# Optimization experiments

Measured on AMD Instinct MI355X. Metric: run time of the kernel, lower is better.

Reference implementation:

```python
import jax, jax.numpy as jnp
import numpy as np

THRESH_FACTOR = 0.7

def _bitlinear(x, w, scale):
    # Ternary quantization of weights: sign(w) masked by |w| > mean(|w|)*0.7,
    # STE in torch means forward value == wq; scale is per-output-row.
    w_abs = jnp.abs(w)
    thr = jnp.mean(w_abs) * THRESH_FACTOR
    wq = jnp.sign(w) * (w_abs > thr).astype(w.dtype)
    w_scaled = wq * scale  # [out, in]
    return jnp.einsum('bsd,od->bso', x, w_scaled)

def setup_inputs() -> dict:
    key = jax.random.key(0)
    k1, k2, k3, k4 = jax.random.split(key, 4)
    dim, hidden = 4096, 16384
    x = jax.random.normal(k1, (2, 2048, dim), dtype=jnp.float32)
    gate_w = jax.random.normal(k2, (hidden, dim), dtype=jnp.float32) / np.sqrt(dim)
    up_w = jax.random.normal(k3, (hidden, dim), dtype=jnp.float32) / np.sqrt(dim)
    down_w = jax.random.normal(k4, (dim, hidden), dtype=jnp.float32) / np.sqrt(hidden)
    return {
        'x': x,
        'gate_w': gate_w, 'gate_scale': jnp.ones((hidden, 1), jnp.float32),
        'up_w': up_w, 'up_scale': jnp.ones((hidden, 1), jnp.float32),
        'down_w': down_w, 'down_scale': jnp.ones((dim, 1), jnp.float32),
    }

def reference(x, gate_w, gate_scale, up_w, up_scale, down_w, down_scale):
    gate = _bitlinear(x, gate_w, gate_scale)      # [B,S,hidden]
    up = _bitlinear(x, up_w, up_scale)            # [B,S,hidden]
    hidden = jax.nn.silu(gate) * up
    out = _bitlinear(hidden, down_w, down_scale)  # [B,S,dim]
    # FakeQuantActivation with bits=8 is an exact identity (bits >= 8 branch)
    return out
```

## Files before the change

kernel.cpp:

```cpp
#include <hip/hip_runtime.h>

typedef __attribute__((ext_vector_type(8))) short short8;
typedef __attribute__((ext_vector_type(4))) float f32x4;

#define AS1 __attribute__((address_space(1)))
#define AS3 __attribute__((address_space(3)))

__device__ __forceinline__ void async_cp16(void* lds_dst, const void* g_src) {
  __builtin_amdgcn_global_load_lds((const AS1 void*)g_src, (AS3 void*)lds_dst, 16, 0, 0);
}

__device__ __forceinline__ unsigned short f2bf(float f) {
  unsigned int x = __float_as_uint(f);
  x += 0x7FFFu + ((x >> 16) & 1u);
  return (unsigned short)(x >> 16);
}

__global__ void k_absmean(const float4* __restrict__ w, int n4, double* __restrict__ out) {
  double s = 0.0;
  int stride = gridDim.x * blockDim.x;
  for (int i = blockIdx.x * blockDim.x + threadIdx.x; i < n4; i += stride) {
    float4 v = w[i];
    s += (double)(fabsf(v.x) + fabsf(v.y) + fabsf(v.z) + fabsf(v.w));
  }
  for (int off = 32; off > 0; off >>= 1) s += __shfl_down(s, off);
  __shared__ double ss[4];
  int lane = threadIdx.x & 63, wid = threadIdx.x >> 6;
  if (lane == 0) ss[wid] = s;
  __syncthreads();
  if (threadIdx.x == 0) atomicAdd(out, ss[0] + ss[1] + ss[2] + ss[3]);
}

__global__ void k_quant_w_dense(const float* __restrict__ w, unsigned short* __restrict__ dst,
                                int nchunks, const double* __restrict__ sum, double inv_n) {
  float thr = (float)(*sum * 0.7 * inv_n);
  int stride = gridDim.x * blockDim.x;
  const float4* w4 = (const float4*)w;
  for (int c = blockIdx.x * blockDim.x + threadIdx.x; c < nchunks; c += stride) {
    float4 a = w4[(size_t)c * 2], b = w4[(size_t)c * 2 + 1];
    float v[8] = {a.x, a.y, a.z, a.w, b.x, b.y, b.z, b.w};
    short8 o;
#pragma unroll
    for (int e = 0; e < 8; e++) {
      unsigned int bits = __float_as_uint(v[e]);
      unsigned short q = (fabsf(v[e]) > thr)
                             ? (unsigned short)(0x3F80u | ((bits >> 16) & 0x8000u))
                             : (unsigned short)0;
      o[e] = (short)q;
    }
    *(short8*)(dst + (size_t)c * 8) = o;
  }
}

__global__ void k_quant_w_inplace(float* __restrict__ w, int nchunks,
                                  const double* __restrict__ sum, double inv_n) {
  float thr = (float)(*sum * 0.7 * inv_n);
  int stride = gridDim.x * blockDim.x;
  for (int c = blockIdx.x * blockDim.x + threadIdx.x; c < nchunks; c += stride) {
    const float4* src = (const float4*)((const char*)w + (size_t)c * 32);
    float4 a = src[0], b = src[1];
    float v[8] = {a.x, a.y, a.z, a.w, b.x, b.y, b.z, b.w};
    short8 o;
#pragma unroll
    for (int e = 0; e < 8; e++) {
      unsigned int bits = __float_as_uint(v[e]);
      unsigned short q = (fabsf(v[e]) > thr)
                             ? (unsigned short)(0x3F80u | ((bits >> 16) & 0x8000u))
                             : (unsigned short)0;
      o[e] = (short)q;
    }
    *(short8*)((char*)w + (size_t)c * 32) = o;
  }
}

__global__ void k_quant_x(const float4* __restrict__ x, unsigned short* __restrict__ xq,
                          int nchunks) {
  int stride = gridDim.x * blockDim.x;
  for (int c = blockIdx.x * blockDim.x + threadIdx.x; c < nchunks; c += stride) {
    float4 a = x[(size_t)c * 2], b = x[(size_t)c * 2 + 1];
    float v[8] = {a.x, a.y, a.z, a.w, b.x, b.y, b.z, b.w};
    short8 o;
#pragma unroll
    for (int e = 0; e < 8; e++) o[e] = (short)f2bf(v[e]);
    *(short8*)(xq + (size_t)c * 8) = o;
  }
}

__global__ __launch_bounds__(256, 2) void k_mlp_gemm1(
    const char* __restrict__ xq, const char* __restrict__ gw, const char* __restrict__ uw,
    const float* __restrict__ gscale, const float* __restrict__ uscale,
    unsigned short* __restrict__ hidden, size_t bRow, int bChunk, int bStep) {
  __shared__ __align__(16) unsigned short sA[4096], sG[4096], sU[4096];
  const int tid = threadIdx.x, lane = tid & 63, wid = tid >> 6;
  const int mt = blockIdx.x & 31, nt = blockIdx.x >> 5;
  const size_t m0 = (size_t)mt * 128, n0 = (size_t)nt * 128;

  const int q0 = wid * 64 + lane, q1 = q0 + 256;
  const int r0 = q0 >> 2, c0 = (q0 & 3) ^ ((q0 >> 3) & 3);
  const int r1 = q1 >> 2, c1 = (q1 & 3) ^ ((q1 >> 3) & 3);

  const char* srcA0 = xq + (m0 + r0) * 8192 + c0 * 16;
  const char* srcA1 = xq + (m0 + r1) * 8192 + c1 * 16;
  const char* srcG0 = gw + (n0 + r0) * bRow + (size_t)c0 * bChunk;
  const char* srcG1 = gw + (n0 + r1) * bRow + (size_t)c1 * bChunk;
  const char* srcU0 = uw + (n0 + r0) * bRow + (size_t)c0 * bChunk;
  const char* srcU1 = uw + (n0 + r1) * bRow + (size_t)c1 * bChunk;

  char* dA0 = (char*)sA + wid * 1024; char* dA1 = dA0 + 4096;
  char* dG0 = (char*)sG + wid * 1024; char* dG1 = dG0 + 4096;
  char* dU0 = (char*)sU + wid * 1024; char* dU1 = dU0 + 4096;

  const int wm = wid >> 1, wn = wid & 1, ln = lane & 15;
  const int slot = ((lane >> 4) ^ ((ln >> 1) & 3)) * 16;
  const char* aBase = (const char*)sA + (size_t)(wm * 64 + ln) * 64 + slot;
  const char* gBase = (const char*)sG + (size_t)(wn * 64 + ln) * 64 + slot;
  const char* uBase = (const char*)sU + (size_t)(wn * 64 + ln) * 64 + slot;

  f32x4 accg[4][4] = {}; f32x4 accu[4][4] = {};

  for (int kt = 0; kt < 4096; kt += 32) {
    async_cp16(dA0, srcA0); async_cp16(dA1, srcA1);
    async_cp16(dG0, srcG0); async_cp16(dG1, srcG1);
    async_cp16(dU0, srcU0); async_cp16(dU1, srcU1);
    srcA0 += 64; srcA1 += 64;
    srcG0 += bStep; srcG1 += bStep; srcU0 += bStep; srcU1 += bStep;
    __syncthreads();
    short8 a[4], bg[4], bu[4];
#pragma unroll
    for (int i = 0; i < 4; i++) {
      a[i]  = *(const short8*)(aBase + i * 1024);
      bg[i] = *(const short8*)(gBase + i * 1024);
      bu[i] = *(const short8*)(uBase + i * 1024);
    }
#pragma unroll
    for (int i = 0; i < 4; i++)
#pragma unroll
      for (int j = 0; j < 4; j++) {
        accg[i][j] = __builtin_amdgcn_mfma_f32_16x16x32_bf16(a[i], bg[j], accg[i][j], 0, 0, 0);
        accu[i][j] = __builtin_amdgcn_mfma_f32_16x16x32_bf16(a[i], bu[j], accu[i][j], 0, 0, 0);
      }
    __syncthreads();
  }

  const int rgrp = lane >> 4;
#pragma unroll
  for (int j = 0; j < 4; j++) {
    int n = (int)n0 + wn * 64 + j * 16 + ln;
    float gs = gscale[n], us = uscale[n];
#pragma unroll
    for (int i = 0; i < 4; i++) {
      int rowb = (int)m0 + wm * 64 + i * 16 + rgrp * 4;
#pragma unroll
      for (int r = 0; r < 4; r++) {
        float g = accg[i][j][r] * gs;
        float u = accu[i][j][r] * us;
        float h = g * (1.0f / (1.0f + __expf(-g))) * u;
        hidden[(size_t)(rowb + r) * 16384 + n] = f2bf(h);
      }
    }
  }
}

__global__ __launch_bounds__(256, 3) void k_mlp_gemm2(
    const char* __restrict__ hq, const char* __restrict__ dw,
    const float* __restrict__ dscale, float* __restrict__ out,
    size_t bRow, int bChunk, int bStep) {
  __shared__ __align__(16) unsigned short sA[4096], sB[4096];
  const int tid = threadIdx.x, lane = tid & 63, wid = tid >> 6;
  const int mt = blockIdx.x & 31, nt = blockIdx.x >> 5;
  const size_t m0 = (size_t)mt * 128, n0 = (size_t)nt * 128;

  const int q0 = wid * 64 + lane, q1 = q0 + 256;
  const int r0 = q0 >> 2, c0 = (q0 & 3) ^ ((q0 >> 3) & 3);
  const int r1 = q1 >> 2, c1 = (q1 & 3) ^ ((q1 >> 3) & 3);

  const char* srcA0 = hq + (m0 + r0) * 32768 + c0 * 16;
  const char* srcA1 = hq + (m0 + r1) * 32768 + c1 * 16;
  const char* srcB0 = dw + (n0 + r0) * bRow + (size_t)c0 * bChunk;
  const char* srcB1 = dw + (n0 + r1) * bRow + (size_t)c1 * bChunk;

  char* dA0 = (char*)sA + wid * 1024; char* dA1 = dA0 + 4096;
  char* dB0 = (char*)sB + wid * 1024; char* dB1 = dB0 + 4096;

  const int wm = wid >> 1, wn = wid & 1, ln = lane & 15;
  const int slot = ((lane >> 4) ^ ((ln >> 1) & 3)) * 16;
  const char* aBase = (const char*)sA + (size_t)(wm * 64 + ln) * 64 + slot;
  const char* bBase = (const char*)sB + (size_t)(wn * 64 + ln) * 64 + slot;

  f32x4 acc[4][4] = {};

  for (int kt = 0; kt < 16384; kt += 32) {
    async_cp16(dA0, srcA0); async_cp16(dA1, srcA1);
    async_cp16(dB0, srcB0); async_cp16(dB1, srcB1);
    srcA0 += 64; srcA1 += 64; srcB0 += bStep; srcB1 += bStep;
    __syncthreads();
    short8 a[4], b[4];
#pragma unroll
    for (int i = 0; i < 4; i++) {
      a[i] = *(const short8*)(aBase + i * 1024);
      b[i] = *(const short8*)(bBase + i * 1024);
    }
#pragma unroll
    for (int i = 0; i < 4; i++)
#pragma unroll
      for (int j = 0; j < 4; j++)
        acc[i][j] = __builtin_amdgcn_mfma_f32_16x16x32_bf16(a[i], b[j], acc[i][j], 0, 0, 0);
    __syncthreads();
  }

  const int rgrp = lane >> 4;
#pragma unroll
  for (int j = 0; j < 4; j++) {
    int n = (int)n0 + wn * 64 + j * 16 + ln;
    float ds = dscale[n];
#pragma unroll
    for (int i = 0; i < 4; i++) {
      int rowb = (int)m0 + wm * 64 + i * 16 + rgrp * 4;
#pragma unroll
      for (int r = 0; r < 4; r++)
        out[(size_t)(rowb + r) * 4096 + n] = acc[i][j][r] * ds;
    }
  }
}

extern "C" void kernel_launch(void* const* d_in, const int* in_sizes, int n_in,
                              void* d_out, int out_size, void* d_ws, size_t ws_size,
                              hipStream_t stream) {
  (void)in_sizes; (void)n_in; (void)out_size;
  const float* x      = (const float*)d_in[0];
  float*       gate_w = (float*)d_in[1];
  const float* gscale = (const float*)d_in[2];
  float*       up_w   = (float*)d_in[3];
  const float* uscale = (const float*)d_in[4];
  float*       down_w = (float*)d_in[5];
  const float* dscale = (const float*)d_in[6];
  float*       out    = (float*)d_out;

  const size_t MB128 = 134217728ull;
  const bool dense = ws_size >= 4 * MB128 + 24;
  unsigned short* hidden = (unsigned short*)d_ws;
  unsigned short* gq = (unsigned short*)((char*)d_ws + 1 * MB128);
  unsigned short* uq = (unsigned short*)((char*)d_ws + 2 * MB128);
  unsigned short* dq = (unsigned short*)((char*)d_ws + 3 * MB128);
  double* sums = (double*)((char*)d_ws + (dense ? 4 * MB128 : MB128));
  unsigned short* xq = (unsigned short*)d_out;

  hipMemsetAsync(sums, 0, 3 * sizeof(double), stream);
  k_absmean<<<4096, 256, 0, stream>>>((const float4*)gate_w, 16777216, sums + 0);
  k_absmean<<<4096, 256, 0, stream>>>((const float4*)up_w,   16777216, sums + 1);
  k_absmean<<<4096, 256, 0, stream>>>((const float4*)down_w, 16777216, sums + 2);

  const double inv_n = 1.0 / 67108864.0;
  k_quant_x<<<2048, 256, 0, stream>>>((const float4*)x, xq, 2097152);

  if (dense) {
    k_quant_w_dense<<<4096, 256, 0, stream>>>(gate_w, gq, 8388608, sums + 0, inv_n);
    k_quant_w_dense<<<4096, 256, 0, stream>>>(up_w,   uq, 8388608, sums + 1, inv_n);
    k_quant_w_dense<<<4096, 256, 0, stream>>>(down_w, dq, 8388608, sums + 2, inv_n);
    k_mlp_gemm1<<<4096, 256, 0, stream>>>((const char*)xq, (const char*)gq, (const char*)uq,
                                          gscale, uscale, hidden, 8192, 16, 64);
    k_mlp_gemm2<<<1024, 256, 0, stream>>>((const char*)hidden, (const char*)dq,
                                          dscale, out, 32768, 16, 64);
  } else {
    k_quant_w_inplace<<<4096, 256, 0, stream>>>(gate_w, 8388608, sums + 0, inv_n);
    k_quant_w_inplace<<<4096, 256, 0, stream>>>(up_w,   8388608, sums + 1, inv_n);
    k_quant_w_inplace<<<4096, 256, 0, stream>>>(down_w, 8388608, sums + 2, inv_n);
    k_mlp_gemm1<<<4096, 256, 0, stream>>>((const char*)xq, (const char*)gate_w,
                                          (const char*)up_w, gscale, uscale, hidden,
                                          16384, 32, 128);
    k_mlp_gemm2<<<1024, 256, 0, stream>>>((const char*)hidden, (const char*)down_w,
                                          dscale, out, 65536, 32, 128);
  }
}
```

Before: 2.760 ms.

## Pipeline GEMMs with 4-stage LDS ring, 8-wave blocks, merge prep kernels

Both GEMMs now use 512-thread blocks with a 128KB four-slot LDS ring buffer, so global-to-LDS async copies run two k-steps ahead. Split barriers with s_waitcnt and s_setprio let MFMA work overlap with loads. Tile shapes grow (gemm1 256x128, gemm2 256x256) and block IDs are swizzled for L2 locality. The separate absmean and quantization kernels are merged into two launches to cut launch overhead. In exchange, the large LDS footprint limits occupancy and raises register pressure, and the hand-tuned waitcnt counts are fragile.

```diff
diff --git a/kernel.cpp b/kernel.cpp
--- a/kernel.cpp
+++ b/kernel.cpp
@@ -6,7 +6,7 @@
 #define AS1 __attribute__((address_space(1)))
 #define AS3 __attribute__((address_space(3)))
 
-__device__ __forceinline__ void async_cp16(void* lds_dst, const void* g_src) {
+__device__ __forceinline__ void async_cp16(char* lds_dst, const char* g_src) {
   __builtin_amdgcn_global_load_lds((const AS1 void*)g_src, (AS3 void*)lds_dst, 16, 0, 0);
 }
 
@@ -16,10 +16,13 @@
   return (unsigned short)(x >> 16);
 }
 
-__global__ void k_absmean(const float4* __restrict__ w, int n4, double* __restrict__ out) {
+__global__ void k_sums(const float4* __restrict__ w0, const float4* __restrict__ w1,
+                       const float4* __restrict__ w2, double* __restrict__ out) {
+  const int seg = blockIdx.x >> 12, bid = blockIdx.x & 4095;
+  const float4* w = (seg == 0) ? w0 : (seg == 1) ? w1 : w2;
   double s = 0.0;
-  int stride = gridDim.x * blockDim.x;
-  for (int i = blockIdx.x * blockDim.x + threadIdx.x; i < n4; i += stride) {
+  const int stride = 4096 * 256;
+  for (int i = bid * 256 + threadIdx.x; i < 16777216; i += stride) {
     float4 v = w[i];
     s += (double)(fabsf(v.x) + fabsf(v.y) + fabsf(v.z) + fabsf(v.w));
   }
@@ -28,199 +31,251 @@
   int lane = threadIdx.x & 63, wid = threadIdx.x >> 6;
   if (lane == 0) ss[wid] = s;
   __syncthreads();
-  if (threadIdx.x == 0) atomicAdd(out, ss[0] + ss[1] + ss[2] + ss[3]);
-}
-
-__global__ void k_quant_w_dense(const float* __restrict__ w, unsigned short* __restrict__ dst,
-                                int nchunks, const double* __restrict__ sum, double inv_n) {
-  float thr = (float)(*sum * 0.7 * inv_n);
-  int stride = gridDim.x * blockDim.x;
-  const float4* w4 = (const float4*)w;
-  for (int c = blockIdx.x * blockDim.x + threadIdx.x; c < nchunks; c += stride) {
-    float4 a = w4[(size_t)c * 2], b = w4[(size_t)c * 2 + 1];
-    float v[8] = {a.x, a.y, a.z, a.w, b.x, b.y, b.z, b.w};
-    short8 o;
-#pragma unroll
-    for (int e = 0; e < 8; e++) {
-      unsigned int bits = __float_as_uint(v[e]);
-      unsigned short q = (fabsf(v[e]) > thr)
-                             ? (unsigned short)(0x3F80u | ((bits >> 16) & 0x8000u))
-                             : (unsigned short)0;
-      o[e] = (short)q;
-    }
-    *(short8*)(dst + (size_t)c * 8) = o;
-  }
-}
-
-__global__ void k_quant_w_inplace(float* __restrict__ w, int nchunks,
-                                  const double* __restrict__ sum, double inv_n) {
-  float thr = (float)(*sum * 0.7 * inv_n);
-  int stride = gridDim.x * blockDim.x;
-  for (int c = blockIdx.x * blockDim.x + threadIdx.x; c < nchunks; c += stride) {
-    const float4* src = (const float4*)((const char*)w + (size_t)c * 32);
-    float4 a = src[0], b = src[1];
-    float v[8] = {a.x, a.y, a.z, a.w, b.x, b.y, b.z, b.w};
-    short8 o;
-#pragma unroll
-    for (int e = 0; e < 8; e++) {
-      unsigned int bits = __float_as_uint(v[e]);
-      unsigned short q = (fabsf(v[e]) > thr)
-                             ? (unsigned short)(0x3F80u | ((bits >> 16) & 0x8000u))
-                             : (unsigned short)0;
-      o[e] = (short)q;
-    }
-    *(short8*)((char*)w + (size_t)c * 32) = o;
-  }
-}
-
-__global__ void k_quant_x(const float4* __restrict__ x, unsigned short* __restrict__ xq,
-                          int nchunks) {
-  int stride = gridDim.x * blockDim.x;
-  for (int c = blockIdx.x * blockDim.x + threadIdx.x; c < nchunks; c += stride) {
-    float4 a = x[(size_t)c * 2], b = x[(size_t)c * 2 + 1];
-    float v[8] = {a.x, a.y, a.z, a.w, b.x, b.y, b.z, b.w};
-    short8 o;
-#pragma unroll
-    for (int e = 0; e < 8; e++) o[e] = (short)f2bf(v[e]);
-    *(short8*)(xq + (size_t)c * 8) = o;
-  }
-}
-
-__global__ __launch_bounds__(256, 2) void k_mlp_gemm1(
+  if (threadIdx.x == 0) atomicAdd(out + seg, ss[0] + ss[1] + ss[2] + ss[3]);
+}
+
+__global__ void k_prep(const float4* __restrict__ x, unsigned short* __restrict__ xq,
+                       float* __restrict__ w0, float* __restrict__ w1, float* __restrict__ w2,
+                       unsigned short* __restrict__ d0, unsigned short* __restrict__ d1,
+                       unsigned short* __restrict__ d2,
+                       const double* __restrict__ sums, double inv_n, int dense) {
+  const int seg = blockIdx.x >> 12;
+  if (seg < 3) {
+    float* w = (seg == 0) ? w0 : (seg == 1) ? w1 : w2;
+    unsigned short* dst = (seg == 0) ? d0 : (seg == 1) ? d1 : d2;
+    const float thr = (float)(sums[seg] * 0.7 * inv_n);
+    const int bid = blockIdx.x & 4095, stride = 4096 * 256;
+    for (int c = bid * 256 + threadIdx.x; c < 8388608; c += stride) {
+      float4 a, b;
+      if (dense) {
+        const float4* w4 = (const float4*)w;
+        a = w4[(size_t)c * 2]; b = w4[(size_t)c * 2 + 1];
+      } else {
+        const float4* src = (const float4*)((const char*)w + (size_t)c * 32);
+        a = src[0]; b = src[1];
+      }
+      float v[8] = {a.x, a.y, a.z, a.w, b.x, b.y, b.z, b.w};
+      short8 o;
+#pragma unroll
+      for (int e = 0; e < 8; e++) {
+        unsigned int bits = __float_as_uint(v[e]);
+        unsigned short q = (fabsf(v[e]) > thr)
+                               ? (unsigned short)(0x3F80u | ((bits >> 16) & 0x8000u))
+                               : (unsigned short)0;
+        o[e] = (short)q;
+      }
+      if (dense) *(short8*)(dst + (size_t)c * 8) = o;
+      else       *(short8*)((char*)w + (size_t)c * 32) = o;
+    }
+  } else {
+    const int bid = blockIdx.x & 4095, stride = 1024 * 256;
+    for (int c = bid * 256 + threadIdx.x; c < 2097152; c += stride) {
+      float4 a = x[(size_t)c * 2], b = x[(size_t)c * 2 + 1];
+      float v[8] = {a.x, a.y, a.z, a.w, b.x, b.y, b.z, b.w};
+      short8 o;
+#pragma unroll
+      for (int e = 0; e < 8; e++) o[e] = (short)f2bf(v[e]);
+      *(short8*)(xq + (size_t)c * 8) = o;
+    }
+  }
+}
+
+
+__global__ __launch_bounds__(512, 2) void k_gemm1_8p(
     const char* __restrict__ xq, const char* __restrict__ gw, const char* __restrict__ uw,
     const float* __restrict__ gscale, const float* __restrict__ uscale,
-    unsigned short* __restrict__ hidden, size_t bRow, int bChunk, int bStep) {
-  __shared__ __align__(16) unsigned short sA[4096], sG[4096], sU[4096];
+    unsigned short* __restrict__ hidden, size_t rowB, int chunkB, int stepB) {
+  __shared__ __align__(16) char lds[131072];
   const int tid = threadIdx.x, lane = tid & 63, wid = tid >> 6;
-  const int mt = blockIdx.x & 31, nt = blockIdx.x >> 5;
-  const size_t m0 = (size_t)mt * 128, n0 = (size_t)nt * 128;
-
-  const int q0 = wid * 64 + lane, q1 = q0 + 256;
-  const int r0 = q0 >> 2, c0 = (q0 & 3) ^ ((q0 >> 3) & 3);
-  const int r1 = q1 >> 2, c1 = (q1 & 3) ^ ((q1 >> 3) & 3);
-
-  const char* srcA0 = xq + (m0 + r0) * 8192 + c0 * 16;
-  const char* srcA1 = xq + (m0 + r1) * 8192 + c1 * 16;
-  const char* srcG0 = gw + (n0 + r0) * bRow + (size_t)c0 * bChunk;
-  const char* srcG1 = gw + (n0 + r1) * bRow + (size_t)c1 * bChunk;
-  const char* srcU0 = uw + (n0 + r0) * bRow + (size_t)c0 * bChunk;
-  const char* srcU1 = uw + (n0 + r1) * bRow + (size_t)c1 * bChunk;
-
-  char* dA0 = (char*)sA + wid * 1024; char* dA1 = dA0 + 4096;
-  char* dG0 = (char*)sG + wid * 1024; char* dG1 = dG0 + 4096;
-  char* dU0 = (char*)sU + wid * 1024; char* dU1 = dU0 + 4096;
+  const int bidp = (blockIdx.x & 7) * 256 + (blockIdx.x >> 3);
+  const int mt = bidp & 15, nt = bidp >> 4;
+  const size_t m0 = (size_t)mt * 256, n0 = (size_t)nt * 128;
+
+  const int sr = tid >> 2;
+  const int sc = (tid & 3) ^ ((sr >> 1) & 3);
+  const char* srcA0 = xq + (m0 + sr) * 8192 + sc * 16;
+  const char* srcA1 = xq + (m0 + 128 + sr) * 8192 + sc * 16;
+  const char* srcG  = gw + (n0 + sr) * rowB + (size_t)sc * chunkB;
+  const char* srcU  = uw + (n0 + sr) * rowB + (size_t)sc * chunkB;
+  const unsigned ldA0 = tid * 16, ldA1 = 8192 + tid * 16;
+  const unsigned ldG = 16384 + tid * 16, ldU = 24576 + tid * 16;
 
   const int wm = wid >> 1, wn = wid & 1, ln = lane & 15;
   const int slot = ((lane >> 4) ^ ((ln >> 1) & 3)) * 16;
-  const char* aBase = (const char*)sA + (size_t)(wm * 64 + ln) * 64 + slot;
-  const char* gBase = (const char*)sG + (size_t)(wn * 64 + ln) * 64 + slot;
-  const char* uBase = (const char*)sU + (size_t)(wn * 64 + ln) * 64 + slot;
+  unsigned aOff[4], gOff[4], uOff[4];
+#pragma unroll
+  for (int i = 0; i < 4; i++) aOff[i] = (wm * 64 + i * 16 + ln) * 64 + slot;
+#pragma unroll
+  for (int j = 0; j < 4; j++) {
+    gOff[j] = 16384 + (wn * 64 + j * 16 + ln) * 64 + slot;
+    uOff[j] = 24576 + (wn * 64 + j * 16 + ln) * 64 + slot;
+  }
 
   f32x4 accg[4][4] = {}; f32x4 accu[4][4] = {};
 
-  for (int kt = 0; kt < 4096; kt += 32) {
-    async_cp16(dA0, srcA0); async_cp16(dA1, srcA1);
-    async_cp16(dG0, srcG0); async_cp16(dG1, srcG1);
-    async_cp16(dU0, srcU0); async_cp16(dU1, srcU1);
-    srcA0 += 64; srcA1 += 64;
-    srcG0 += bStep; srcG1 += bStep; srcU0 += bStep; srcU1 += bStep;
-    __syncthreads();
-    short8 a[4], bg[4], bu[4];
-#pragma unroll
-    for (int i = 0; i < 4; i++) {
-      a[i]  = *(const short8*)(aBase + i * 1024);
-      bg[i] = *(const short8*)(gBase + i * 1024);
-      bu[i] = *(const short8*)(uBase + i * 1024);
-    }
-#pragma unroll
-    for (int i = 0; i < 4; i++)
-#pragma unroll
-      for (int j = 0; j < 4; j++) {
-        accg[i][j] = __builtin_amdgcn_mfma_f32_16x16x32_bf16(a[i], bg[j], accg[i][j], 0, 0, 0);
-        accu[i][j] = __builtin_amdgcn_mfma_f32_16x16x32_bf16(a[i], bu[j], accu[i][j], 0, 0, 0);
-      }
-    __syncthreads();
-  }
-
-  const int rgrp = lane >> 4;
+#define G1_STP1(BB) { async_cp16(lds + (BB) + ldA0, srcA0); async_cp16(lds + (BB) + ldG, srcG); }
+#define G1_STP2(BB) { async_cp16(lds + (BB) + ldA1, srcA1); async_cp16(lds + (BB) + ldU, srcU); }
+#define G1_ADV()    { srcA0 += 64; srcA1 += 64; srcG += stepB; srcU += stepB; }
+
+  G1_STP1(0) G1_STP2(0) G1_ADV();
+  G1_STP1(32768) G1_STP2(32768) G1_ADV();
+  asm volatile("s_waitcnt vmcnt(4)" ::: "memory");
+  __builtin_amdgcn_s_barrier();
+
+  for (int q = 0; q < 32; ++q) {
+#pragma unroll
+    for (int j4 = 0; j4 < 4; ++j4) {
+      const int t = q * 4 + j4;
+      const unsigned RB = (unsigned)(t & 3) * 32768;
+      const unsigned SB = (unsigned)((t + 2) & 3) * 32768;
+      const bool st = t < 126;
+      short8 a[4], g[4];
+#pragma unroll
+      for (int i = 0; i < 4; i++) a[i] = *(const short8*)(lds + RB + aOff[i]);
+#pragma unroll
+      for (int j = 0; j < 4; j++) g[j] = *(const short8*)(lds + RB + gOff[j]);
+      if (st) { G1_STP1(SB); }
+      __builtin_amdgcn_s_barrier();
+      __builtin_amdgcn_s_setprio(1);
+#pragma unroll
+      for (int i = 0; i < 4; i++)
+#pragma unroll
+        for (int j = 0; j < 4; j++)
+          accg[i][j] = __builtin_amdgcn_mfma_f32_16x16x32_bf16(a[i], g[j], accg[i][j], 0, 0, 0);
+      __builtin_amdgcn_s_setprio(0);
+      short8 u[4];
+#pragma unroll
+      for (int j = 0; j < 4; j++) u[j] = *(const short8*)(lds + RB + uOff[j]);
+      if (st) { G1_STP2(SB); }
+      G1_ADV();
+      if (st) { asm volatile("s_waitcnt vmcnt(4)" ::: "memory"); }
+      else    { asm volatile("s_waitcnt vmcnt(0)" ::: "memory"); }
+      __builtin_amdgcn_s_barrier();
+      __builtin_amdgcn_s_setprio(1);
+#pragma unroll
+      for (int i = 0; i < 4; i++)
+#pragma unroll
+        for (int j = 0; j < 4; j++)
+          accu[i][j] = __builtin_amdgcn_mfma_f32_16x16x32_bf16(a[i], u[j], accu[i][j], 0, 0, 0);
+      __builtin_amdgcn_s_setprio(0);
+    }
+  }
+
+  const int rg = lane >> 4;
 #pragma unroll
   for (int j = 0; j < 4; j++) {
     int n = (int)n0 + wn * 64 + j * 16 + ln;
     float gs = gscale[n], us = uscale[n];
 #pragma unroll
     for (int i = 0; i < 4; i++) {
-      int rowb = (int)m0 + wm * 64 + i * 16 + rgrp * 4;
+      int row = (int)m0 + wm * 64 + i * 16 + rg * 4;
 #pragma unroll
       for (int r = 0; r < 4; r++) {
-        float g = accg[i][j][r] * gs;
-        float u = accu[i][j][r] * us;
-        float h = g * (1.0f / (1.0f + __expf(-g))) * u;
-        hidden[(size_t)(rowb + r) * 16384 + n] = f2bf(h);
+        float gv = accg[i][j][r] * gs;
+        float uv = accu[i][j][r] * us;
+        float h = gv * (1.0f / (1.0f + __expf(-gv))) * uv;
+        hidden[(size_t)(row + r) * 16384 + n] = f2bf(h);
       }
     }
   }
-}
-
-__global__ __launch_bounds__(256, 3) void k_mlp_gemm2(
+#undef G1_STP1
+#undef G1_STP2
+#undef G1_ADV
+}
+
+__global__ __launch_bounds__(512, 2) void k_gemm2_8p(
     const char* __restrict__ hq, const char* __restrict__ dw,
     const float* __restrict__ dscale, float* __restrict__ out,
-    size_t bRow, int bChunk, int bStep) {
-  __shared__ __align__(16) unsigned short sA[4096], sB[4096];
+    size_t rowB, int chunkB, int stepB) {
+  __shared__ __align__(16) char lds[131072];
   const int tid = threadIdx.x, lane = tid & 63, wid = tid >> 6;
-  const int mt = blockIdx.x & 31, nt = blockIdx.x >> 5;
-  const size_t m0 = (size_t)mt * 128, n0 = (size_t)nt * 128;
-
-  const int q0 = wid * 64 + lane, q1 = q0 + 256;
-  const int r0 = q0 >> 2, c0 = (q0 & 3) ^ ((q0 >> 3) & 3);
-  const int r1 = q1 >> 2, c1 = (q1 & 3) ^ ((q1 >> 3) & 3);
-
-  const char* srcA0 = hq + (m0 + r0) * 32768 + c0 * 16;
-  const char* srcA1 = hq + (m0 + r1) * 32768 + c1 * 16;
-  const char* srcB0 = dw + (n0 + r0) * bRow + (size_t)c0 * bChunk;
-  const char* srcB1 = dw + (n0 + r1) * bRow + (size_t)c1 * bChunk;
-
-  char* dA0 = (char*)sA + wid * 1024; char* dA1 = dA0 + 4096;
-  char* dB0 = (char*)sB + wid * 1024; char* dB1 = dB0 + 4096;
-
-  const int wm = wid >> 1, wn = wid & 1, ln = lane & 15;
+  const int bidp = (blockIdx.x & 7) * 32 + (blockIdx.x >> 3);
+  const int mt = bidp & 15, nt = bidp >> 4;
+  const size_t m0 = (size_t)mt * 256, n0 = (size_t)nt * 256;
+
+  const int sr = tid >> 2;
+  const int sc = (tid & 3) ^ ((sr >> 1) & 3);
+  const char* srcA0 = hq + (m0 + sr) * 32768 + sc * 16;
+  const char* srcA1 = hq + (m0 + 128 + sr) * 32768 + sc * 16;
+  const char* srcB0 = dw + (n0 + sr) * rowB + (size_t)sc * chunkB;
+  const char* srcB1 = dw + (n0 + 128 + sr) * rowB + (size_t)sc * chunkB;
+  const unsigned ldA0 = tid * 16, ldA1 = 8192 + tid * 16;
+  const unsigned ldB0 = 16384 + tid * 16, ldB1 = 24576 + tid * 16;
+
+  const int wm = wid >> 2, wn = wid & 3, ln = lane & 15;
   const int slot = ((lane >> 4) ^ ((ln >> 1) & 3)) * 16;
-  const char* aBase = (const char*)sA + (size_t)(wm * 64 + ln) * 64 + slot;
-  const char* bBase = (const char*)sB + (size_t)(wn * 64 + ln) * 64 + slot;
-
-  f32x4 acc[4][4] = {};
-
-  for (int kt = 0; kt < 16384; kt += 32) {
-    async_cp16(dA0, srcA0); async_cp16(dA1, srcA1);
-    async_cp16(dB0, srcB0); async_cp16(dB1, srcB1);
-    srcA0 += 64; srcA1 += 64; srcB0 += bStep; srcB1 += bStep;
-    __syncthreads();
-    short8 a[4], b[4];
-#pragma unroll
-    for (int i = 0; i < 4; i++) {
-      a[i] = *(const short8*)(aBase + i * 1024);
-      b[i] = *(const short8*)(bBase + i * 1024);
-    }
-#pragma unroll
-    for (int i = 0; i < 4; i++)
-#pragma unroll
-      for (int j = 0; j < 4; j++)
-        acc[i][j] = __builtin_amdgcn_mfma_f32_16x16x32_bf16(a[i], b[j], acc[i][j], 0, 0, 0);
-    __syncthreads();
-  }
-
-  const int rgrp = lane >> 4;
+  unsigned aOff[8], bOff[4];
+#pragma unroll
+  for (int i = 0; i < 8; i++) aOff[i] = (wm * 128 + i * 16 + ln) * 64 + slot;
+#pragma unroll
+  for (int j = 0; j < 4; j++) bOff[j] = 16384 + (wn * 64 + j * 16 + ln) * 64 + slot;
+
+  f32x4 acc[8][4] = {};
+
+#define G2_STP1(BB) { async_cp16(lds + (BB) + ldA0, srcA0); async_cp16(lds + (BB) + ldB0, srcB0); }
+#define G2_STP2(BB) { async_cp16(lds + (BB) + ldA1, srcA1); async_cp16(lds + (BB) + ldB1, srcB1); }
+#define G2_ADV()    { srcA0 += 64; srcA1 += 64; srcB0 += stepB; srcB1 += stepB; }
+
+  G2_STP1(0) G2_STP2(0) G2_ADV();
+  G2_STP1(32768) G2_STP2(32768) G2_ADV();
+  asm volatile("s_waitcnt vmcnt(4)" ::: "memory");
+  __builtin_amdgcn_s_barrier();
+
+  for (int q = 0; q < 128; ++q) {
+#pragma unroll
+    for (int j4 = 0; j4 < 4; ++j4) {
+      const int t = q * 4 + j4;
+      const unsigned RB = (unsigned)(t & 3) * 32768;
+      const unsigned SB = (unsigned)((t + 2) & 3) * 32768;
+      const bool st = t < 510;
+      short8 a0[4], b[4];
+#pragma unroll
+      for (int i = 0; i < 4; i++) a0[i] = *(const short8*)(lds + RB + aOff[i]);
+#pragma unroll
+      for (int j = 0; j < 4; j++) b[j] = *(const short8*)(lds + RB + bOff[j]);
+      if (st) { G2_STP1(SB); }
+      __builtin_amdgcn_s_barrier();
+      __builtin_amdgcn_s_setprio(1);
+#pragma unroll
+      for (int i = 0; i < 4; i++)
+#pragma unroll
+        for (int j = 0; j < 4; j++)
+          acc[i][j] = __builtin_amdgcn_mfma_f32_16x16x32_bf16(a0[i], b[j], acc[i][j], 0, 0, 0);
+      __builtin_amdgcn_s_setprio(0);
+      short8 a1[4];
+#pragma unroll
+      for (int i = 0; i < 4; i++) a1[i] = *(const short8*)(lds + RB + aOff[4 + i]);
+      if (st) { G2_STP2(SB); }
+      G2_ADV();
+      if (st) { asm volatile("s_waitcnt vmcnt(4)" ::: "memory"); }
+      else    { asm volatile("s_waitcnt vmcnt(0)" ::: "memory"); }
+      __builtin_amdgcn_s_barrier();
+      __builtin_amdgcn_s_setprio(1);
+#pragma unroll
+      for (int i = 0; i < 4; i++)
+#pragma unroll
+        for (int j = 0; j < 4; j++)
+          acc[4 + i][j] = __builtin_amdgcn_mfma_f32_16x16x32_bf16(a1[i], b[j], acc[4 + i][j], 0, 0, 0);
+      __builtin_amdgcn_s_setprio(0);
+    }
+  }
+
+  const int rg = lane >> 4;
 #pragma unroll
   for (int j = 0; j < 4; j++) {
     int n = (int)n0 + wn * 64 + j * 16 + ln;
     float ds = dscale[n];
 #pragma unroll
-    for (int i = 0; i < 4; i++) {
-      int rowb = (int)m0 + wm * 64 + i * 16 + rgrp * 4;
+    for (int i = 0; i < 8; i++) {
+      int row = (int)m0 + wm * 128 + i * 16 + rg * 4;
 #pragma unroll
       for (int r = 0; r < 4; r++)
-        out[(size_t)(rowb + r) * 4096 + n] = acc[i][j][r] * ds;
-    }
-  }
+        out[(size_t)(row + r) * 4096 + n] = acc[i][j][r] * ds;
+    }
+  }
+#undef G2_STP1
+#undef G2_STP2
+#undef G2_ADV
 }
 
 extern "C" void kernel_launch(void* const* d_in, const int* in_sizes, int n_in,
@@ -246,29 +301,23 @@
   unsigned short* xq = (unsigned short*)d_out;
 
   hipMemsetAsync(sums, 0, 3 * sizeof(double), stream);
-  k_absmean<<<4096, 256, 0, stream>>>((const float4*)gate_w, 16777216, sums + 0);
-  k_absmean<<<4096, 256, 0, stream>>>((const float4*)up_w,   16777216, sums + 1);
-  k_absmean<<<4096, 256, 0, stream>>>((const float4*)down_w, 16777216, sums + 2);
+  k_sums<<<12288, 256, 0, stream>>>((const float4*)gate_w, (const float4*)up_w,
+                                    (const float4*)down_w, sums);
 
   const double inv_n = 1.0 / 67108864.0;
-  k_quant_x<<<2048, 256, 0, stream>>>((const float4*)x, xq, 2097152);
+  k_prep<<<13312, 256, 0, stream>>>((const float4*)x, xq, gate_w, up_w, down_w,
+                                    gq, uq, dq, sums, inv_n, dense ? 1 : 0);
 
   if (dense) {
-    k_quant_w_dense<<<4096, 256, 0, stream>>>(gate_w, gq, 8388608, sums + 0, inv_n);
-    k_quant_w_dense<<<4096, 256, 0, stream>>>(up_w,   uq, 8388608, sums + 1, inv_n);
-    k_quant_w_dense<<<4096, 256, 0, stream>>>(down_w, dq, 8388608, sums + 2, inv_n);
-    k_mlp_gemm1<<<4096, 256, 0, stream>>>((const char*)xq, (const char*)gq, (const char*)uq,
-                                          gscale, uscale, hidden, 8192, 16, 64);
-    k_mlp_gemm2<<<1024, 256, 0, stream>>>((const char*)hidden, (const char*)dq,
-                                          dscale, out, 32768, 16, 64);
+    k_gemm1_8p<<<2048, 512, 0, stream>>>((const char*)xq, (const char*)gq, (const char*)uq,
+                                         gscale, uscale, hidden, 8192, 16, 64);
+    k_gemm2_8p<<<256, 512, 0, stream>>>((const char*)hidden, (const char*)dq,
+                                        dscale, out, 32768, 16, 64);
   } else {
-    k_quant_w_inplace<<<4096, 256, 0, stream>>>(gate_w, 8388608, sums + 0, inv_n);
-    k_quant_w_inplace<<<4096, 256, 0, stream>>>(up_w,   8388608, sums + 1, inv_n);
-    k_quant_w_inplace<<<4096, 256, 0, stream>>>(down_w, 8388608, sums + 2, inv_n);
-    k_mlp_gemm1<<<4096, 256, 0, stream>>>((const char*)xq, (const char*)gate_w,
-                                          (const char*)up_w, gscale, uscale, hidden,
-                                          16384, 32, 128);
-    k_mlp_gemm2<<<1024, 256, 0, stream>>>((const char*)hidden, (const char*)down_w,
-                                          dscale, out, 65536, 32, 128);
-  }
-}
+    k_gemm1_8p<<<2048, 512, 0, stream>>>((const char*)xq, (const char*)gate_w,
+                                         (const char*)up_w, gscale, uscale, hidden,
+                                         16384, 32, 128);
+    k_gemm2_8p<<<256, 512, 0, stream>>>((const char*)hidden, (const char*)down_w,
+                                        dscale, out, 65536, 32, 128);
+  }
+}
```

Measured after the change: 2.503 ms. 1.1x faster.
